# Kernel optimization log

Measured on AMD Instinct MI355X. Metric: run time of the kernel, lower is better.

## Reference

```python
import jax, jax.numpy as jnp
import numpy as np

EPS = 1e-5

def layer_norm(x, w, b):
    # normalize over last two dims [N, H]
    mean = jnp.mean(x, axis=(-2, -1), keepdims=True)
    var = jnp.var(x, axis=(-2, -1), keepdims=True)
    return (x - mean) * jax.lax.rsqrt(var + EPS) * w + b

def lg_conv(x, edge_index, num_nodes):
    # LightGCN conv: symmetric-normalized neighbor sum (no self loops)
    src, dst = edge_index[0], edge_index[1]
    deg = jnp.zeros((num_nodes,), x.dtype).at[dst].add(1.0)
    dinv = jnp.where(deg > 0, jax.lax.rsqrt(jnp.maximum(deg, 1.0)), 0.0)
    norm = dinv[src] * dinv[dst]                      # [E]
    msgs = x[:, :, src, :] * norm[None, None, :, None]  # [B,P,E,H]
    return jnp.zeros_like(x).at[:, :, dst, :].add(msgs)

def setup_inputs() -> dict:
    key = jax.random.key(0)
    ks = jax.random.split(key, 4)
    B, P, N, H = 16, 12, 2048, 64
    E = 16384
    x = jax.random.normal(ks[0], (B, P, N, H), dtype=jnp.float32)
    edge_index = jax.random.randint(ks[1], (2, E), 0, N, dtype=jnp.int64)
    g_norm_w = jnp.ones((N, H), jnp.float32)
    g_norm_b = jnp.zeros((N, H), jnp.float32)
    t_norm_w = jnp.ones((N, H), jnp.float32)
    t_norm_b = jnp.zeros((N, H), jnp.float32)
    bound = 1.0 / np.sqrt(P)  # Conv2d default init range
    conv_w = jax.random.uniform(ks[2], (P, P), jnp.float32, -bound, bound)
    conv_b = jax.random.uniform(ks[3], (P,), jnp.float32, -bound, bound)
    return {"x": x, "edge_index": edge_index,
            "g_norm_w": g_norm_w, "g_norm_b": g_norm_b,
            "t_norm_w": t_norm_w, "t_norm_b": t_norm_b,
            "conv_w": conv_w, "conv_b": conv_b}

def reference(x, edge_index, g_norm_w, g_norm_b, t_norm_w, t_norm_b, conv_w, conv_b):
    N = x.shape[2]
    h = layer_norm(x, g_norm_w, g_norm_b)
    h = lg_conv(h, edge_index, N)
    h = layer_norm(h, t_norm_w, t_norm_b)
    # 1x1 Conv2d over channels = periods: [B,P,N,H] -> [B,Q,N,H]
    out = jnp.einsum('qp,bpnh->bqnh', conv_w, h) + conv_b[None, :, None, None]
    return out
```

## Files before the change

kernel.cpp:

```cpp
#include <hip/hip_runtime.h>

#define B_ 16
#define P_ 12
#define N_ 2048
#define H_ 64
#define E_ 16384
#define NH_ (N_*H_)
#define NG_ (B_*P_)

__global__ __launch_bounds__(1024) void k_stats_csr(const float* __restrict__ x,
                                                    const int* __restrict__ ew,
                                                    float* __restrict__ mean1,
                                                    float* __restrict__ rstd1,
                                                    int* __restrict__ rowPtr,
                                                    int* __restrict__ csrSrc,
                                                    float* __restrict__ csrW) {
    __shared__ int   sDeg[N_];
    __shared__ int   sA[N_];
    __shared__ int   sB[N_];
    __shared__ float sDinv[N_];
    __shared__ int   sFlag;
    __shared__ float ls[16], lq[16];
    int tid = threadIdx.x;
    if (blockIdx.x < NG_) {
        int g = blockIdx.x;
        const float4* xg = (const float4*)(x + (size_t)g * NH_);
        float s = 0.f, q = 0.f;
        #pragma unroll 8
        for (int i = 0; i < 32; ++i) {
            float4 v = xg[i*1024 + tid];
            s += v.x + v.y + v.z + v.w;
            q += v.x*v.x + v.y*v.y + v.z*v.z + v.w*v.w;
        }
        for (int off = 32; off; off >>= 1) { s += __shfl_down(s, off); q += __shfl_down(q, off); }
        int wid = tid >> 6, lane = tid & 63;
        if (!lane) { ls[wid] = s; lq[wid] = q; }
        __syncthreads();
        if (!tid) {
            float S = 0.f, Q = 0.f;
            #pragma unroll
            for (int i = 0; i < 16; ++i) { S += ls[i]; Q += lq[i]; }
            float m = S * (1.0f/NH_);
            float v = Q * (1.0f/NH_) - m*m;
            mean1[g] = m;
            rstd1[g] = rsqrtf(v + 1e-5f);
        }
        return;
    }
    if (!tid) sFlag = 1;
    for (int i = tid; i < N_; i += 1024) sDeg[i] = 0;
    __syncthreads();
    if (tid < 256) { if (ew[2*tid+1] != 0) atomicAnd(&sFlag, 0); }
    __syncthreads();
    int is64 = sFlag;
    for (int e = tid; e < E_; e += 1024) {
        int dst = is64 ? ew[2*(E_+e)] : ew[E_+e];
        atomicAdd(&sDeg[dst], 1);
    }
    __syncthreads();
    for (int i = tid; i < N_; i += 1024) {
        int d = sDeg[i];
        sDinv[i] = d > 0 ? rsqrtf((float)d) : 0.f;
        sA[i] = d;
    }
    __syncthreads();
    int* in = sA; int* out = sB;
    for (int st = 1; st < N_; st <<= 1) {
        for (int i = tid; i < N_; i += 1024) {
            int v = in[i];
            if (i >= st) v += in[i-st];
            out[i] = v;
        }
        __syncthreads();
        int* t = in; in = out; out = t;
    }
    for (int i = tid; i < N_; i += 1024) {
        int excl = in[i] - sDeg[i];
        rowPtr[i] = excl;
        out[i] = excl;
    }
    if (!tid) rowPtr[N_] = E_;
    __syncthreads();
    for (int e = tid; e < E_; e += 1024) {
        int src = is64 ? ew[2*e]       : ew[e];
        int dst = is64 ? ew[2*(E_+e)]  : ew[E_+e];
        int pos = atomicAdd(&out[dst], 1);
        csrSrc[pos] = src;
        csrW[pos] = sDinv[src] * sDinv[dst];
    }
}

__global__ __launch_bounds__(64) void k_finalize(const float* __restrict__ partials, int cnt,
                                                 float* __restrict__ mean, float* __restrict__ rstd) {
    int g = blockIdx.x, lane = threadIdx.x;
    float s = 0.f, q = 0.f;
    for (int i = lane; i < cnt; i += 64) {
        s += partials[(g*cnt+i)*2];
        q += partials[(g*cnt+i)*2+1];
    }
    for (int off = 32; off; off >>= 1) { s += __shfl_down(s, off); q += __shfl_down(q, off); }
    if (!lane) {
        float m = s * (1.0f/NH_);
        float v = q * (1.0f/NH_) - m*m;
        mean[g] = m;
        rstd[g] = rsqrtf(v + 1e-5f);
    }
}

__global__ __launch_bounds__(256) void k_gather(const float* __restrict__ x,
                                                const float* __restrict__ gw,
                                                const float* __restrict__ gb,
                                                const float* __restrict__ mean1,
                                                const float* __restrict__ rstd1,
                                                const int* __restrict__ rowPtr,
                                                const int* __restrict__ csrSrc,
                                                const float* __restrict__ csrW,
                                                float* __restrict__ h2,
                                                float* __restrict__ partials ) {
    int b     = blockIdx.x & 15;
    int chunk = blockIdx.x >> 4;
    int wid = threadIdx.x >> 6, lane = threadIdx.x & 63;
    __shared__ float s_rs[P_], s_mrs[P_];
    __shared__ float red[4][P_][2];
    if (threadIdx.x < P_) {
        float m = mean1[b*P_ + threadIdx.x], r = rstd1[b*P_ + threadIdx.x];
        s_rs[threadIdx.x] = r; s_mrs[threadIdx.x] = m*r;
    }
    __syncthreads();
    const float* xb = x + (size_t)b * P_ * NH_;
    float sp[P_], qp[P_];
    #pragma unroll
    for (int p = 0; p < P_; ++p) { sp[p] = 0.f; qp[p] = 0.f; }
    #pragma unroll
    for (int i = 0; i < 4; ++i) {
        int n  = chunk*16 + wid*4 + i;
        int r0 = rowPtr[n], r1 = rowPtr[n+1];
        float acc[P_];
        #pragma unroll
        for (int p = 0; p < P_; ++p) acc[p] = 0.f;
        float An = 0.f, Bn = 0.f;
        if (r0 < r1) {
            int   src = csrSrc[r0];
            float w   = csrW[r0];
            for (int j = r0; j < r1; ++j) {
                int   ro  = src*H_ + lane;
                float gwv = gw[ro];
                float gbv = gb[ro];
                int   nsrc = 0; float nw = 0.f;
                if (j+1 < r1) { nsrc = csrSrc[j+1]; nw = csrW[j+1]; }
                float t = w * gwv;
                Bn += t;
                An += w * gbv;
                #pragma unroll
                for (int p = 0; p < P_; ++p)
                    acc[p] += t * xb[(size_t)p*NH_ + ro];
                src = nsrc; w = nw;
            }
        }
        size_t ob = (size_t)b*P_*NH_ + (size_t)n*H_ + lane;
        #pragma unroll
        for (int p = 0; p < P_; ++p) {
            float val = s_rs[p]*acc[p] - s_mrs[p]*Bn + An;
            h2[ob + (size_t)p*NH_] = val;
            sp[p] += val; qp[p] += val*val;
        }
    }
    #pragma unroll
    for (int p = 0; p < P_; ++p) {
        float s = sp[p], q = qp[p];
        for (int off = 32; off; off >>= 1) { s += __shfl_down(s, off); q += __shfl_down(q, off); }
        if (!lane) { red[wid][p][0] = s; red[wid][p][1] = q; }
    }
    __syncthreads();
    if (threadIdx.x < P_*2) {
        int p = threadIdx.x >> 1, c = threadIdx.x & 1;
        float v = red[0][p][c] + red[1][p][c] + red[2][p][c] + red[3][p][c];
        partials[(((b*P_ + p) << 7) + chunk)*2 + c] = v;
    }
}

__global__ __launch_bounds__(256) void k_mix(float* __restrict__ h2,
                                             const float* __restrict__ tw,
                                             const float* __restrict__ tb,
                                             const float* __restrict__ cw,
                                             const float* __restrict__ cb,
                                             const float* __restrict__ mean2,
                                             const float* __restrict__ rstd2) {
    __shared__ float scw[P_*P_], scb[P_], sm[P_], sr[P_], srow[P_];
    int b     = blockIdx.x >> 7;
    int chunk = blockIdx.x & 127;
    int tid   = threadIdx.x;
    if (tid < P_*P_) scw[tid] = cw[tid];
    if (tid < P_) {
        scb[tid] = cb[tid];
        sm[tid]  = mean2[b*P_ + tid];
        sr[tid]  = rstd2[b*P_ + tid];
    }
    __syncthreads();
    if (tid < P_) {
        float rs = 0.f;
        #pragma unroll
        for (int p = 0; p < P_; ++p) rs += scw[tid*P_ + p];
        srow[tid] = rs;
    }
    __syncthreads();
    int elem4 = chunk*256 + tid;
    size_t base = (size_t)b * P_ * NH_;
    float4 v[P_];
    #pragma unroll
    for (int p = 0; p < P_; ++p) {
        float4 t = *(const float4*)(h2 + base + (size_t)p*NH_ + (size_t)elem4*4);
        float m = sm[p], r = sr[p];
        v[p].x = (t.x-m)*r; v[p].y = (t.y-m)*r; v[p].z = (t.z-m)*r; v[p].w = (t.w-m)*r;
    }
    float4 tw4 = *(const float4*)(tw + (size_t)elem4*4);
    float4 tb4 = *(const float4*)(tb + (size_t)elem4*4);
    #pragma unroll
    for (int q = 0; q < P_; ++q) {
        float4 a = {0.f,0.f,0.f,0.f};
        #pragma unroll
        for (int p = 0; p < P_; ++p) {
            float c = scw[q*P_ + p];
            a.x += c*v[p].x; a.y += c*v[p].y; a.z += c*v[p].z; a.w += c*v[p].w;
        }
        float rb = srow[q], cbq = scb[q];
        float4 o;
        o.x = tw4.x*a.x + tb4.x*rb + cbq;
        o.y = tw4.y*a.y + tb4.y*rb + cbq;
        o.z = tw4.z*a.z + tb4.z*rb + cbq;
        o.w = tw4.w*a.w + tb4.w*rb + cbq;
        *(float4*)(h2 + base + (size_t)q*NH_ + (size_t)elem4*4) = o;
    }
}

extern "C" void kernel_launch(void* const* d_in, const int* in_sizes, int n_in,
                              void* d_out, int out_size, void* d_ws, size_t ws_size,
                              hipStream_t stream) {
    const float* x  = (const float*)d_in[0];
    const int*   ew = (const int*)d_in[1];
    const float* gw = (const float*)d_in[2];
    const float* gb = (const float*)d_in[3];
    const float* tw = (const float*)d_in[4];
    const float* tb = (const float*)d_in[5];
    const float* cw = (const float*)d_in[6];
    const float* cb = (const float*)d_in[7];
    float* out = (float*)d_out;
    float* wf  = (float*)d_ws;

    float* mean1  = wf + 0;
    float* rstd1  = wf + 192;
    float* mean2  = wf + 384;
    float* rstd2  = wf + 576;
    float* pC     = wf + 768;
    int*   rowPtr = (int*)(wf + 49920);
    int*   csrSrc = (int*)(wf + 51972);
    float* csrW   = wf + 68356;

    k_stats_csr<<<NG_ + 1, 1024, 0, stream>>>(x, ew, mean1, rstd1, rowPtr, csrSrc, csrW);
    k_gather<<<B_*128, 256, 0, stream>>>(x, gw, gb, mean1, rstd1,
                                         rowPtr, csrSrc, csrW, out, pC);
    k_finalize<<<NG_, 64, 0, stream>>>(pC, 128, mean2, rstd2);
    k_mix<<<B_*128, 256, 0, stream>>>(out, tw, tb, cw, cb, mean2, rstd2);
}
```

Measured before the change: 357.4 us.

## Split gather kernel over period halves and reorder blocks for L2 locality

The gather kernel now handles 6 of the 12 periods per block and launches twice as many blocks. The block index is remapped so that concurrently running blocks cover 8 batches and one period half, which shrinks the working set of x rows held in cache at a time. The software prefetch of the next CSR entry is dropped in favour of a plain loop. In exchange, the weight and bias gathers (gw/gb) and the CSR reads are repeated per half, and there is less ILP per thread.

```diff
diff --git a/kernel.cpp b/kernel.cpp
--- a/kernel.cpp
+++ b/kernel.cpp
@@ -107,6 +107,7 @@
     }
 }
 
+#define PH_ 6
 __global__ __launch_bounds__(256) void k_gather(const float* __restrict__ x,
                                                 const float* __restrict__ gw,
                                                 const float* __restrict__ gb,
@@ -117,65 +118,62 @@
                                                 const float* __restrict__ csrW,
                                                 float* __restrict__ h2,
                                                 float* __restrict__ partials ) {
-    int b     = blockIdx.x & 15;
-    int chunk = blockIdx.x >> 4;
+    int blk   = blockIdx.x & 1023;
+    int phase = blockIdx.x >> 10;
+    int bh    = phase & 1, ph = phase >> 1;
+    int b     = bh*8 + (blk & 7);
+    int chunk = blk >> 3;
+    int p0    = ph*PH_;
     int wid = threadIdx.x >> 6, lane = threadIdx.x & 63;
-    __shared__ float s_rs[P_], s_mrs[P_];
-    __shared__ float red[4][P_][2];
-    if (threadIdx.x < P_) {
-        float m = mean1[b*P_ + threadIdx.x], r = rstd1[b*P_ + threadIdx.x];
+    __shared__ float s_rs[PH_], s_mrs[PH_];
+    __shared__ float red[4][PH_][2];
+    if (threadIdx.x < PH_) {
+        float m = mean1[b*P_ + p0 + threadIdx.x], r = rstd1[b*P_ + p0 + threadIdx.x];
         s_rs[threadIdx.x] = r; s_mrs[threadIdx.x] = m*r;
     }
     __syncthreads();
-    const float* xb = x + (size_t)b * P_ * NH_;
-    float sp[P_], qp[P_];
-    #pragma unroll
-    for (int p = 0; p < P_; ++p) { sp[p] = 0.f; qp[p] = 0.f; }
+    const float* xb = x + ((size_t)b*P_ + p0) * NH_;
+    float sp[PH_], qp[PH_];
+    #pragma unroll
+    for (int p = 0; p < PH_; ++p) { sp[p] = 0.f; qp[p] = 0.f; }
     #pragma unroll
     for (int i = 0; i < 4; ++i) {
         int n  = chunk*16 + wid*4 + i;
         int r0 = rowPtr[n], r1 = rowPtr[n+1];
-        float acc[P_];
-        #pragma unroll
-        for (int p = 0; p < P_; ++p) acc[p] = 0.f;
+        float acc[PH_];
+        #pragma unroll
+        for (int p = 0; p < PH_; ++p) acc[p] = 0.f;
         float An = 0.f, Bn = 0.f;
-        if (r0 < r1) {
-            int   src = csrSrc[r0];
-            float w   = csrW[r0];
-            for (int j = r0; j < r1; ++j) {
-                int   ro  = src*H_ + lane;
-                float gwv = gw[ro];
-                float gbv = gb[ro];
-                int   nsrc = 0; float nw = 0.f;
-                if (j+1 < r1) { nsrc = csrSrc[j+1]; nw = csrW[j+1]; }
-                float t = w * gwv;
-                Bn += t;
-                An += w * gbv;
-                #pragma unroll
-                for (int p = 0; p < P_; ++p)
-                    acc[p] += t * xb[(size_t)p*NH_ + ro];
-                src = nsrc; w = nw;
-            }
-        }
-        size_t ob = (size_t)b*P_*NH_ + (size_t)n*H_ + lane;
-        #pragma unroll
-        for (int p = 0; p < P_; ++p) {
+        for (int j = r0; j < r1; ++j) {
+            int   src = csrSrc[j];
+            float w   = csrW[j];
+            int   ro  = src*H_ + lane;
+            float t   = w * gw[ro];
+            Bn += t;
+            An += w * gb[ro];
+            #pragma unroll
+            for (int p = 0; p < PH_; ++p)
+                acc[p] += t * xb[(size_t)p*NH_ + ro];
+        }
+        size_t ob = ((size_t)b*P_ + p0)*NH_ + (size_t)n*H_ + lane;
+        #pragma unroll
+        for (int p = 0; p < PH_; ++p) {
             float val = s_rs[p]*acc[p] - s_mrs[p]*Bn + An;
             h2[ob + (size_t)p*NH_] = val;
             sp[p] += val; qp[p] += val*val;
         }
     }
     #pragma unroll
-    for (int p = 0; p < P_; ++p) {
+    for (int p = 0; p < PH_; ++p) {
         float s = sp[p], q = qp[p];
         for (int off = 32; off; off >>= 1) { s += __shfl_down(s, off); q += __shfl_down(q, off); }
         if (!lane) { red[wid][p][0] = s; red[wid][p][1] = q; }
     }
     __syncthreads();
-    if (threadIdx.x < P_*2) {
+    if (threadIdx.x < PH_*2) {
         int p = threadIdx.x >> 1, c = threadIdx.x & 1;
         float v = red[0][p][c] + red[1][p][c] + red[2][p][c] + red[3][p][c];
-        partials[(((b*P_ + p) << 7) + chunk)*2 + c] = v;
+        partials[(((b*P_ + p0 + p) << 7) + chunk)*2 + c] = v;
     }
 }
 
@@ -257,8 +255,8 @@
     float* csrW   = wf + 68356;
 
     k_stats_csr<<<NG_ + 1, 1024, 0, stream>>>(x, ew, mean1, rstd1, rowPtr, csrSrc, csrW);
-    k_gather<<<B_*128, 256, 0, stream>>>(x, gw, gb, mean1, rstd1,
-                                         rowPtr, csrSrc, csrW, out, pC);
+    k_gather<<<4096, 256, 0, stream>>>(x, gw, gb, mean1, rstd1,
+                                       rowPtr, csrSrc, csrW, out, pC);
     k_finalize<<<NG_, 64, 0, stream>>>(pC, 128, mean2, rstd2);
     k_mix<<<B_*128, 256, 0, stream>>>(out, tw, tb, cw, cb, mean2, rstd2);
 }
```

After: 386.0 us. +8.0%, slower.

## Precompute per-node affine terms, interleave gathers, split stats, fuse finalize into mix

Applied to the files above, without the earlier changes.

The per-node affine terms A and B (weighted sums of gb and gw over neighbours) no longer depend on batch, so a new k_ab kernel computes them once instead of once per batch inside the gather. The gather loop now runs four nodes' edge lists together to raise memory-level parallelism. Edge source and weight are packed into an int2 pair, so each edge needs one load. First-pass stats are split across four blocks per group for more parallelism, and the second-pass finalize kernel is folded into k_mix, which removes one launch but repeats that reduction in every mix block.

```diff
diff --git a/kernel.cpp b/kernel.cpp
--- a/kernel.cpp
+++ b/kernel.cpp
@@ -8,13 +8,20 @@
 #define NH_ (N_*H_)
 #define NG_ (B_*P_)
 
+#define WS_MEAN1  0
+#define WS_RSTD1  192
+#define WS_PA     384
+#define WS_AG     2048
+#define WS_BG     133120
+#define WS_PC     264192
+#define WS_ROWPTR 313344
+#define WS_PAIR   315400
+
 __global__ __launch_bounds__(1024) void k_stats_csr(const float* __restrict__ x,
                                                     const int* __restrict__ ew,
-                                                    float* __restrict__ mean1,
-                                                    float* __restrict__ rstd1,
+                                                    float* __restrict__ pA,
                                                     int* __restrict__ rowPtr,
-                                                    int* __restrict__ csrSrc,
-                                                    float* __restrict__ csrW) {
+                                                    int2* __restrict__ pair) {
     __shared__ int   sDeg[N_];
     __shared__ int   sA[N_];
     __shared__ int   sB[N_];
@@ -22,13 +29,14 @@
     __shared__ int   sFlag;
     __shared__ float ls[16], lq[16];
     int tid = threadIdx.x;
-    if (blockIdx.x < NG_) {
-        int g = blockIdx.x;
+    if (blockIdx.x < 768) {
+        int g = blockIdx.x >> 2, seg = blockIdx.x & 3;
         const float4* xg = (const float4*)(x + (size_t)g * NH_);
         float s = 0.f, q = 0.f;
-        #pragma unroll 8
-        for (int i = 0; i < 32; ++i) {
-            float4 v = xg[i*1024 + tid];
+        int base = seg * 8192;
+        #pragma unroll
+        for (int i = 0; i < 8; ++i) {
+            float4 v = xg[base + i*1024 + tid];
             s += v.x + v.y + v.z + v.w;
             q += v.x*v.x + v.y*v.y + v.z*v.z + v.w*v.w;
         }
@@ -40,10 +48,8 @@
             float S = 0.f, Q = 0.f;
             #pragma unroll
             for (int i = 0; i < 16; ++i) { S += ls[i]; Q += lq[i]; }
-            float m = S * (1.0f/NH_);
-            float v = Q * (1.0f/NH_) - m*m;
-            mean1[g] = m;
-            rstd1[g] = rsqrtf(v + 1e-5f);
+            pA[blockIdx.x*2]   = S;
+            pA[blockIdx.x*2+1] = Q;
         }
         return;
     }
@@ -85,38 +91,60 @@
         int src = is64 ? ew[2*e]       : ew[e];
         int dst = is64 ? ew[2*(E_+e)]  : ew[E_+e];
         int pos = atomicAdd(&out[dst], 1);
-        csrSrc[pos] = src;
-        csrW[pos] = sDinv[src] * sDinv[dst];
-    }
-}
-
-__global__ __launch_bounds__(64) void k_finalize(const float* __restrict__ partials, int cnt,
-                                                 float* __restrict__ mean, float* __restrict__ rstd) {
-    int g = blockIdx.x, lane = threadIdx.x;
-    float s = 0.f, q = 0.f;
-    for (int i = lane; i < cnt; i += 64) {
-        s += partials[(g*cnt+i)*2];
-        q += partials[(g*cnt+i)*2+1];
-    }
-    for (int off = 32; off; off >>= 1) { s += __shfl_down(s, off); q += __shfl_down(q, off); }
-    if (!lane) {
-        float m = s * (1.0f/NH_);
-        float v = q * (1.0f/NH_) - m*m;
-        mean[g] = m;
-        rstd[g] = rsqrtf(v + 1e-5f);
-    }
+        int2 pr; pr.x = src; pr.y = __float_as_int(sDinv[src] * sDinv[dst]);
+        pair[pos] = pr;
+    }
+}
+
+__global__ __launch_bounds__(256) void k_ab(const float* __restrict__ gw,
+                                            const float* __restrict__ gb,
+                                            const int* __restrict__ rowPtr,
+                                            const int2* __restrict__ pair,
+                                            const float* __restrict__ pA,
+                                            float* __restrict__ Ag,
+                                            float* __restrict__ Bg,
+                                            float* __restrict__ mean1,
+                                            float* __restrict__ rstd1) {
+    int tid = threadIdx.x;
+    if (blockIdx.x == 512) {
+        if (tid < NG_) {
+            float s = 0.f, q = 0.f;
+            #pragma unroll
+            for (int i = 0; i < 4; ++i) {
+                s += pA[(tid*4+i)*2];
+                q += pA[(tid*4+i)*2+1];
+            }
+            float m = s * (1.0f/NH_);
+            float v = q * (1.0f/NH_) - m*m;
+            mean1[tid] = m;
+            rstd1[tid] = rsqrtf(v + 1e-5f);
+        }
+        return;
+    }
+    int wid = tid >> 6, lane = tid & 63;
+    int n = blockIdx.x*4 + wid;
+    int j = rowPtr[n], e = rowPtr[n+1];
+    float A = 0.f, Bv = 0.f;
+    for (; j < e; ++j) {
+        int2 pr = pair[j];
+        float w = __int_as_float(pr.y);
+        int ro = pr.x*H_ + lane;
+        A  += w * gb[ro];
+        Bv += w * gw[ro];
+    }
+    Ag[n*H_ + lane] = A;
+    Bg[n*H_ + lane] = Bv;
 }
 
 __global__ __launch_bounds__(256) void k_gather(const float* __restrict__ x,
-                                                const float* __restrict__ gw,
-                                                const float* __restrict__ gb,
                                                 const float* __restrict__ mean1,
                                                 const float* __restrict__ rstd1,
                                                 const int* __restrict__ rowPtr,
-                                                const int* __restrict__ csrSrc,
-                                                const float* __restrict__ csrW,
+                                                const int2* __restrict__ pair,
+                                                const float* __restrict__ Ag,
+                                                const float* __restrict__ Bg,
                                                 float* __restrict__ h2,
-                                                float* __restrict__ partials ) {
+                                                float* __restrict__ pC) {
     int b     = blockIdx.x & 15;
     int chunk = blockIdx.x >> 4;
     int wid = threadIdx.x >> 6, lane = threadIdx.x & 63;
@@ -128,42 +156,56 @@
     }
     __syncthreads();
     const float* xb = x + (size_t)b * P_ * NH_;
+    int n0 = chunk*16 + wid*4;
+    int r0 = rowPtr[n0], r1 = rowPtr[n0+1], r2 = rowPtr[n0+2],
+        r3 = rowPtr[n0+3], r4 = rowPtr[n0+4];
+    int j0 = r0, e0 = r1, j1 = r1, e1 = r2, j2 = r2, e2 = r3, j3 = r3, e3 = r4;
+    float A0 = Ag[(n0+0)*H_+lane], B0 = Bg[(n0+0)*H_+lane];
+    float A1 = Ag[(n0+1)*H_+lane], B1 = Bg[(n0+1)*H_+lane];
+    float A2 = Ag[(n0+2)*H_+lane], B2 = Bg[(n0+2)*H_+lane];
+    float A3 = Ag[(n0+3)*H_+lane], B3 = Bg[(n0+3)*H_+lane];
+    float ac0[P_], ac1[P_], ac2[P_], ac3[P_];
+    #pragma unroll
+    for (int p = 0; p < P_; ++p) { ac0[p]=0.f; ac1[p]=0.f; ac2[p]=0.f; ac3[p]=0.f; }
+    while ((j0 < e0) | (j1 < e1) | (j2 < e2) | (j3 < e3)) {
+        if (j0 < e0) {
+            int2 pr = pair[j0++]; float w = __int_as_float(pr.y); int ro = pr.x*H_ + lane;
+            #pragma unroll
+            for (int p = 0; p < P_; ++p) ac0[p] += w * xb[(size_t)p*NH_ + ro];
+        }
+        if (j1 < e1) {
+            int2 pr = pair[j1++]; float w = __int_as_float(pr.y); int ro = pr.x*H_ + lane;
+            #pragma unroll
+            for (int p = 0; p < P_; ++p) ac1[p] += w * xb[(size_t)p*NH_ + ro];
+        }
+        if (j2 < e2) {
+            int2 pr = pair[j2++]; float w = __int_as_float(pr.y); int ro = pr.x*H_ + lane;
+            #pragma unroll
+            for (int p = 0; p < P_; ++p) ac2[p] += w * xb[(size_t)p*NH_ + ro];
+        }
+        if (j3 < e3) {
+            int2 pr = pair[j3++]; float w = __int_as_float(pr.y); int ro = pr.x*H_ + lane;
+            #pragma unroll
+            for (int p = 0; p < P_; ++p) ac3[p] += w * xb[(size_t)p*NH_ + ro];
+        }
+    }
     float sp[P_], qp[P_];
     #pragma unroll
     for (int p = 0; p < P_; ++p) { sp[p] = 0.f; qp[p] = 0.f; }
-    #pragma unroll
-    for (int i = 0; i < 4; ++i) {
-        int n  = chunk*16 + wid*4 + i;
-        int r0 = rowPtr[n], r1 = rowPtr[n+1];
-        float acc[P_];
-        #pragma unroll
-        for (int p = 0; p < P_; ++p) acc[p] = 0.f;
-        float An = 0.f, Bn = 0.f;
-        if (r0 < r1) {
-            int   src = csrSrc[r0];
-            float w   = csrW[r0];
-            for (int j = r0; j < r1; ++j) {
-                int   ro  = src*H_ + lane;
-                float gwv = gw[ro];
-                float gbv = gb[ro];
-                int   nsrc = 0; float nw = 0.f;
-                if (j+1 < r1) { nsrc = csrSrc[j+1]; nw = csrW[j+1]; }
-                float t = w * gwv;
-                Bn += t;
-                An += w * gbv;
-                #pragma unroll
-                for (int p = 0; p < P_; ++p)
-                    acc[p] += t * xb[(size_t)p*NH_ + ro];
-                src = nsrc; w = nw;
-            }
-        }
-        size_t ob = (size_t)b*P_*NH_ + (size_t)n*H_ + lane;
-        #pragma unroll
-        for (int p = 0; p < P_; ++p) {
-            float val = s_rs[p]*acc[p] - s_mrs[p]*Bn + An;
-            h2[ob + (size_t)p*NH_] = val;
-            sp[p] += val; qp[p] += val*val;
-        }
+    size_t obb = (size_t)b*P_*NH_ + (size_t)n0*H_ + lane;
+    #pragma unroll
+    for (int p = 0; p < P_; ++p) {
+        size_t op = obb + (size_t)p*NH_;
+        float v0 = s_rs[p]*ac0[p] - s_mrs[p]*B0 + A0;
+        float v1 = s_rs[p]*ac1[p] - s_mrs[p]*B1 + A1;
+        float v2 = s_rs[p]*ac2[p] - s_mrs[p]*B2 + A2;
+        float v3 = s_rs[p]*ac3[p] - s_mrs[p]*B3 + A3;
+        h2[op]        = v0;
+        h2[op + H_]   = v1;
+        h2[op + 2*H_] = v2;
+        h2[op + 3*H_] = v3;
+        sp[p] += v0+v1+v2+v3;
+        qp[p] += v0*v0+v1*v1+v2*v2+v3*v3;
     }
     #pragma unroll
     for (int p = 0; p < P_; ++p) {
@@ -175,7 +217,7 @@
     if (threadIdx.x < P_*2) {
         int p = threadIdx.x >> 1, c = threadIdx.x & 1;
         float v = red[0][p][c] + red[1][p][c] + red[2][p][c] + red[3][p][c];
-        partials[(((b*P_ + p) << 7) + chunk)*2 + c] = v;
+        pC[(((b*P_ + p) << 7) + chunk)*2 + c] = v;
     }
 }
 
@@ -184,17 +226,26 @@
                                              const float* __restrict__ tb,
                                              const float* __restrict__ cw,
                                              const float* __restrict__ cb,
-                                             const float* __restrict__ mean2,
-                                             const float* __restrict__ rstd2) {
+                                             const float* __restrict__ pC) {
     __shared__ float scw[P_*P_], scb[P_], sm[P_], sr[P_], srow[P_];
     int b     = blockIdx.x >> 7;
     int chunk = blockIdx.x & 127;
     int tid   = threadIdx.x;
+    int wid   = tid >> 6, lane = tid & 63;
     if (tid < P_*P_) scw[tid] = cw[tid];
-    if (tid < P_) {
-        scb[tid] = cb[tid];
-        sm[tid]  = mean2[b*P_ + tid];
-        sr[tid]  = rstd2[b*P_ + tid];
+    if (tid < P_) scb[tid] = cb[tid];
+    #pragma unroll
+    for (int pp = 0; pp < 3; ++pp) {
+        int p = wid*3 + pp;
+        int g = b*P_ + p;
+        float s = pC[((g<<7) + lane)*2]     + pC[((g<<7) + 64 + lane)*2];
+        float q = pC[((g<<7) + lane)*2 + 1] + pC[((g<<7) + 64 + lane)*2 + 1];
+        for (int off = 32; off; off >>= 1) { s += __shfl_down(s, off); q += __shfl_down(q, off); }
+        if (!lane) {
+            float m = s * (1.0f/NH_);
+            sm[p] = m;
+            sr[p] = rsqrtf(q * (1.0f/NH_) - m*m + 1e-5f);
+        }
     }
     __syncthreads();
     if (tid < P_) {
@@ -247,18 +298,17 @@
     float* out = (float*)d_out;
     float* wf  = (float*)d_ws;
 
-    float* mean1  = wf + 0;
-    float* rstd1  = wf + 192;
-    float* mean2  = wf + 384;
-    float* rstd2  = wf + 576;
-    float* pC     = wf + 768;
-    int*   rowPtr = (int*)(wf + 49920);
-    int*   csrSrc = (int*)(wf + 51972);
-    float* csrW   = wf + 68356;
-
-    k_stats_csr<<<NG_ + 1, 1024, 0, stream>>>(x, ew, mean1, rstd1, rowPtr, csrSrc, csrW);
-    k_gather<<<B_*128, 256, 0, stream>>>(x, gw, gb, mean1, rstd1,
-                                         rowPtr, csrSrc, csrW, out, pC);
-    k_finalize<<<NG_, 64, 0, stream>>>(pC, 128, mean2, rstd2);
-    k_mix<<<B_*128, 256, 0, stream>>>(out, tw, tb, cw, cb, mean2, rstd2);
-}
+    float* mean1  = wf + WS_MEAN1;
+    float* rstd1  = wf + WS_RSTD1;
+    float* pA     = wf + WS_PA;
+    float* Ag     = wf + WS_AG;
+    float* Bg     = wf + WS_BG;
+    float* pC     = wf + WS_PC;
+    int*   rowPtr = (int*)(wf + WS_ROWPTR);
+    int2*  pair   = (int2*)(wf + WS_PAIR);
+
+    k_stats_csr<<<769, 1024, 0, stream>>>(x, ew, pA, rowPtr, pair);
+    k_ab<<<513, 256, 0, stream>>>(gw, gb, rowPtr, pair, pA, Ag, Bg, mean1, rstd1);
+    k_gather<<<2048, 256, 0, stream>>>(x, mean1, rstd1, rowPtr, pair, Ag, Bg, out, pC);
+    k_mix<<<2048, 256, 0, stream>>>(out, tw, tb, cw, cb, pC);
+}
```

After: 379.8 us. 6.3% more time.
